# Performance work log

Measured on AMD Instinct MI355X. Metric: run time of the kernel, lower is better.

## Reference

```python
import jax, jax.numpy as jnp
import numpy as np

B, S, D = 8, 2048, 1024
H = 4
K = D // 2          # expand_k = 0.5 -> key dim 512
V = D               # expand_v = 1.0 -> value dim 1024
DK, DV = K // H, V // H   # 128, 256
LOW_RANK = 16
GATE_LOGIT_NORM = 16.0
EPS = 1e-5
MLP_H = 4 * D


def _layernorm(x, g, b):
    mu = jnp.mean(x, axis=-1, keepdims=True)
    var = jnp.mean(jnp.square(x - mu), axis=-1, keepdims=True)
    return (x - mu) * jax.lax.rsqrt(var + EPS) * g + b


def _rmsnorm(x, w):
    ms = jnp.mean(jnp.square(x), axis=-1, keepdims=True)
    return x * jax.lax.rsqrt(ms + EPS) * w


def _gla(xn, Wq, Wk, Wv, Wg, Wgk1, Wgk2, bgk, gnorm_w, Wo):
    # projections ([B,S,D] @ [D,*]); weights stored as [in, out]
    q = (xn @ Wq).reshape(B, S, H, DK) * (DK ** -0.5)
    k = (xn @ Wk).reshape(B, S, H, DK)
    v = (xn @ Wv).reshape(B, S, H, DV)
    gk = jax.nn.log_sigmoid(xn @ Wgk1 @ Wgk2 + bgk) / GATE_LOGIT_NORM
    gk = gk.reshape(B, S, H, DK)

    def step(state, inp):
        qt, kt, vt, gt = inp                     # [B,H,DK], [B,H,DK], [B,H,DV], [B,H,DK]
        state = jnp.exp(gt)[..., None] * state + kt[..., None] * vt[..., None, :]
        ot = jnp.einsum('bhk,bhkv->bhv', qt, state)
        return state, ot

    init = jnp.zeros((B, H, DK, DV), xn.dtype)
    xs = (q.transpose(1, 0, 2, 3), k.transpose(1, 0, 2, 3),
          v.transpose(1, 0, 2, 3), gk.transpose(1, 0, 2, 3))
    _, o = jax.lax.scan(step, init, xs)          # o: [S,B,H,DV]
    o = o.transpose(1, 0, 2, 3)                  # [B,S,H,DV]

    g = (xn @ Wg).reshape(B, S, H, DV)
    o = _rmsnorm(o, gnorm_w) * g * jax.nn.sigmoid(g)   # RMSNorm + swish output gate
    return o.reshape(B, S, V) @ Wo


def setup_inputs() -> dict:
    key = jax.random.key(0)
    ks = jax.random.split(key, 16)
    sd = 0.02
    return {
        'x': jax.random.normal(ks[0], (B, S, D), jnp.float32),
        'ln1_g': jnp.ones((D,), jnp.float32),
        'ln1_b': jnp.zeros((D,), jnp.float32),
        'Wq': jax.random.normal(ks[1], (D, K), jnp.float32) * sd,
        'Wk': jax.random.normal(ks[2], (D, K), jnp.float32) * sd,
        'Wv': jax.random.normal(ks[3], (D, V), jnp.float32) * sd,
        'Wg': jax.random.normal(ks[4], (D, V), jnp.float32) * sd,
        'Wgk1': jax.random.normal(ks[5], (D, LOW_RANK), jnp.float32) * sd,
        'Wgk2': jax.random.normal(ks[6], (LOW_RANK, K), jnp.float32) * sd,
        'bgk': jnp.zeros((K,), jnp.float32),
        'gnorm_w': jnp.ones((DV,), jnp.float32),
        'Wo': jax.random.normal(ks[7], (V, D), jnp.float32) * sd,
        'ln2_g': jnp.ones((D,), jnp.float32),
        'ln2_b': jnp.zeros((D,), jnp.float32),
        'W1': jax.random.normal(ks[8], (D, MLP_H), jnp.float32) * sd,
        'b1': jnp.zeros((MLP_H,), jnp.float32),
        'W2': jax.random.normal(ks[9], (MLP_H, D), jnp.float32) * sd,
        'b2': jnp.zeros((D,), jnp.float32),
    }


def reference(x, ln1_g, ln1_b, Wq, Wk, Wv, Wg, Wgk1, Wgk2, bgk, gnorm_w, Wo,
              ln2_g, ln2_b, W1, b1, W2, b2):
    # pre-norm GLA block, eval mode (dropout = identity)
    attn_out = _gla(_layernorm(x, ln1_g, ln1_b), Wq, Wk, Wv, Wg, Wgk1, Wgk2, bgk, gnorm_w, Wo)
    x = x + attn_out
    h = _layernorm(x, ln2_g, ln2_b)
    h = jax.nn.gelu(h @ W1 + b1, approximate=False) @ W2 + b2
    return x + h
```

## Files before the change

kernel.cpp:

```cpp
#include <hip/hip_runtime.h>
#include <stdint.h>


typedef unsigned short u16t;
typedef __attribute__((ext_vector_type(8))) short bf16x8;
typedef __attribute__((ext_vector_type(4))) float f32x4;
typedef __attribute__((ext_vector_type(4))) unsigned short u16x4;

__device__ __forceinline__ float bf2f(unsigned short u){ union{unsigned int i; float f;} v; v.i=((unsigned int)u)<<16; return v.f; }
__device__ __forceinline__ unsigned short f2bf(float f){ union{unsigned int i; float f;} v; v.f=f; unsigned int r=v.i+0x7FFFu+((v.i>>16)&1u); return (unsigned short)(r>>16); }
__device__ __forceinline__ f32x4 cvt4(u16x4 u){ f32x4 r; r[0]=bf2f(u[0]); r[1]=bf2f(u[1]); r[2]=bf2f(u[2]); r[3]=bf2f(u[3]); return r; }
__device__ __forceinline__ u16x4 pack4(f32x4 f){ u16x4 r; r[0]=f2bf(f[0]); r[1]=f2bf(f[1]); r[2]=f2bf(f[2]); r[3]=f2bf(f[3]); return r; }

__device__ __forceinline__ float gelu_f(float t){
  const float t3 = t*t*t;
  const float y = 2.3021183f*t + 0.10295465f*t3;
  const float e = __builtin_amdgcn_exp2f(y);
  return t - t*__builtin_amdgcn_rcpf(e + 1.f);
}

__device__ __forceinline__ void gload_lds16(const unsigned short* g, unsigned short* l)
{
  __builtin_amdgcn_global_load_lds(
      (const __attribute__((address_space(1))) unsigned int*)g,
      (__attribute__((address_space(3))) unsigned int*)l,
      16, 0, 0);
}

__global__ void k_transpose_multi(const float* __restrict__ Wq, const float* __restrict__ Wk,
                                  const float* __restrict__ Wv, const float* __restrict__ Wg,
                                  const float* __restrict__ Wo, const float* __restrict__ W1,
                                  const float* __restrict__ W2,
                                  unsigned short* __restrict__ WPT, unsigned short* __restrict__ WOT,
                                  unsigned short* __restrict__ W1T, unsigned short* __restrict__ W2T)
{
  __shared__ float tile[32][33];
  int bid = blockIdx.x;
  const float* src; unsigned short* dst; int Kin, N, nx;
  if      (bid < 512)  { src=Wq; dst=WPT;                          Kin=1024; N=512;  nx=16;  }
  else if (bid < 1024) { src=Wk; dst=WPT+(size_t)512*1024;         Kin=1024; N=512;  nx=16;  bid-=512;  }
  else if (bid < 2048) { src=Wv; dst=WPT+(size_t)1024*1024;        Kin=1024; N=1024; nx=32;  bid-=1024; }
  else if (bid < 3072) { src=Wg; dst=WPT+(size_t)2048*1024;        Kin=1024; N=1024; nx=32;  bid-=2048; }
  else if (bid < 4096) { src=Wo; dst=WOT;                          Kin=1024; N=1024; nx=32;  bid-=3072; }
  else if (bid < 8192) { src=W1; dst=W1T;                          Kin=1024; N=4096; nx=128; bid-=4096; }
  else                 { src=W2; dst=W2T;                          Kin=4096; N=1024; nx=32;  bid-=8192; }
  const int n0 = (bid % nx)*32, k0 = (bid / nx)*32;
  const int tx = threadIdx.x, ty = threadIdx.y;
  #pragma unroll
  for (int i = 0; i < 4; ++i)
    tile[ty + i*8][tx] = src[(size_t)(k0 + ty + i*8)*N + n0 + tx];
  __syncthreads();
  #pragma unroll
  for (int i = 0; i < 4; ++i)
    dst[(size_t)(n0 + ty + i*8)*Kin + k0 + tx] = f2bf(tile[tx][ty + i*8]);
}

__global__ void k_wgk(const float* __restrict__ Wgk1, const float* __restrict__ Wgk2, unsigned short* __restrict__ dstT)
{
  const int idx = blockIdx.x*256 + threadIdx.x;
  const int i = idx & 1023, j = idx >> 10;
  float s = 0.f;
  #pragma unroll
  for (int r = 0; r < 16; ++r) s += Wgk1[i*16 + r] * Wgk2[r*512 + j];
  dstT[(size_t)j*1024 + i] = f2bf(s);
}

__global__ void k_vtrans(const unsigned short* __restrict__ proj, unsigned short* __restrict__ vtg)
{
  __shared__ unsigned short tile[32][33];
  const int tt = blockIdx.x, dvt = blockIdx.y, bh = blockIdx.z;
  const int b = bh >> 2, h = bh & 3;
  const int tx = threadIdx.x, ty = threadIdx.y;
  #pragma unroll
  for (int i = 0; i < 4; ++i)
    tile[ty + i*8][tx] = proj[((size_t)b*2048 + tt*32 + ty + i*8)*3584 + 1024 + h*256 + dvt*32 + tx];
  __syncthreads();
  #pragma unroll
  for (int i = 0; i < 4; ++i)
    vtg[((size_t)bh*256 + dvt*32 + ty + i*8)*2048 + tt*32 + tx] = tile[tx][ty + i*8];
}

__global__ __launch_bounds__(256) void k_layernorm(const float* __restrict__ x, const float* __restrict__ g,
                                                   const float* __restrict__ b, unsigned short* __restrict__ out)
{
  const int row = blockIdx.x, tid = threadIdx.x;
  const float4 xv = *(const float4*)&x[(size_t)row*1024 + tid*4];
  float s  = xv.x + xv.y + xv.z + xv.w;
  float sq = xv.x*xv.x + xv.y*xv.y + xv.z*xv.z + xv.w*xv.w;
  #pragma unroll
  for (int o = 32; o > 0; o >>= 1) { s += __shfl_xor(s, o); sq += __shfl_xor(sq, o); }
  __shared__ float red[8];
  const int w = tid >> 6;
  if ((tid & 63) == 0) { red[w] = s; red[4 + w] = sq; }
  __syncthreads();
  s  = red[0] + red[1] + red[2] + red[3];
  sq = red[4] + red[5] + red[6] + red[7];
  const float mu = s * (1.f/1024.f);
  const float var = sq * (1.f/1024.f) - mu*mu;
  const float rs = rsqrtf(var + 1e-5f);
  float xe[4] = {xv.x, xv.y, xv.z, xv.w};
  u16x4 o4;
  #pragma unroll
  for (int i = 0; i < 4; ++i) {
    const int c = tid*4 + i;
    o4[i] = f2bf((xe[i] - mu) * rs * g[c] + b[c]);
  }
  *(u16x4*)&out[(size_t)row*1024 + tid*4] = o4;
}

template<int EPI>
__global__ __launch_bounds__(512, 2)
void gemm256(const unsigned short* __restrict__ A, const unsigned short* __restrict__ Bt,
             int N, int K,
             float* outF, unsigned short* outH,
             const float* resid, const float* bias)
{
  __shared__ __align__(16) unsigned short lds[65536];
  const int tid = threadIdx.x;
  const int lane = tid & 63, w = tid >> 6;
  const int wr = w >> 2, wc = w & 3;
  const int l15 = lane & 15, lq = lane >> 4;

  const int nwg = gridDim.x * gridDim.y;
  const int bid = blockIdx.y * gridDim.x + blockIdx.x;
  const int q = nwg >> 3, r = nwg & 7;
  const int xcd = bid & 7, lid = bid >> 3;
  const int sw = (xcd < r ? xcd*(q+1) : r*(q+1) + (xcd - r)*q) + lid;
  const int row0 = (sw / gridDim.x) * 256;
  const int col0 = (sw % gridDim.x) * 256;

  const int rA_ = tid >> 3;
  const int cswz = 8 * ((tid & 7) ^ (rA_ & 7));
  const unsigned short* baseA[2][2];
  const unsigned short* baseB[2][2];
  #pragma unroll
  for (int h = 0; h < 2; ++h)
    #pragma unroll
    for (int L = 0; L < 2; ++L) {
      baseA[h][L] = A  + (size_t)(row0 + h*128 + L*64 + rA_) * K + cswz;
      baseB[h][L] = Bt + (size_t)(col0 + h*128 + L*64 + rA_) * K + cswz;
    }

  const int NT = K >> 6;
  const int NI = NT >> 1;

  f32x4 acc[8][4];
  #pragma unroll
  for (int m = 0; m < 8; ++m)
    #pragma unroll
    for (int n = 0; n < 4; ++n) { acc[m][n][0]=0.f; acc[m][n][1]=0.f; acc[m][n][2]=0.f; acc[m][n][3]=0.f; }

  bf16x8 af[4][2];
  bf16x8 bfr[2][2][2];

  #define STAGE(CH, T)                                                         \
    {                                                                          \
      const int tt = ((T) < NT) ? (T) : (T) - 2;                               \
      const int dbase = (tt & 1) * 32768 + (CH) * 8192;                        \
      const int ktt = tt << 6;                                                 \
      _Pragma("unroll")                                                        \
      for (int L = 0; L < 2; ++L) {                                            \
        const unsigned short* gp =                                             \
            ((CH) < 2 ? baseA[(CH) & 1][L] : baseB[(CH) & 1][L]) + ktt;        \
        gload_lds16(gp, (unsigned short*)&lds[dbase + L*4096 + w*512]);        \
      }                                                                        \
    }

  #define DS_A(CB)                                                             \
    { _Pragma("unroll")                                                        \
      for (int mm = 0; mm < 4; ++mm) {                                         \
        const int rl = wr*64 + mm*16 + l15;                                    \
        const int co = (l15 & 7) * 8;                                          \
        af[mm][0] = *(const bf16x8*)&lds[(CB) + rl*64 + ((lq*8) ^ co)];        \
        af[mm][1] = *(const bf16x8*)&lds[(CB) + rl*64 + ((32 + lq*8) ^ co)];   \
      } }

  #define DS_B(CB, QN)                                                         \
    { _Pragma("unroll")                                                        \
      for (int nn = 0; nn < 2; ++nn) {                                         \
        const int rl = wc*32 + nn*16 + l15;                                    \
        const int co = (l15 & 7) * 8;                                          \
        bfr[QN][nn][0] = *(const bf16x8*)&lds[(CB) + (2+(QN))*8192 + rl*64 + ((lq*8) ^ co)];      \
        bfr[QN][nn][1] = *(const bf16x8*)&lds[(CB) + (2+(QN))*8192 + rl*64 + ((32 + lq*8) ^ co)]; \
      } }

  #define PRE_MFMA()                                                           \
    { __builtin_amdgcn_s_barrier();                                            \
      asm volatile("s_waitcnt lgkmcnt(0)" ::: "memory");                       \
      __builtin_amdgcn_sched_barrier(0); }

  #define MMA(QM, QN)                                                          \
    { __builtin_amdgcn_s_setprio(1);                                           \
      _Pragma("unroll")                                                        \
      for (int mm = 0; mm < 4; ++mm)                                           \
        _Pragma("unroll")                                                      \
        for (int nn = 0; nn < 2; ++nn) {                                       \
          acc[(QM)*4+mm][(QN)*2+nn] = __builtin_amdgcn_mfma_f32_16x16x32_bf16( \
              af[mm][0], bfr[QN][nn][0], acc[(QM)*4+mm][(QN)*2+nn], 0, 0, 0);  \
          acc[(QM)*4+mm][(QN)*2+nn] = __builtin_amdgcn_mfma_f32_16x16x32_bf16( \
              af[mm][1], bfr[QN][nn][1], acc[(QM)*4+mm][(QN)*2+nn], 0, 0, 0);  \
        }                                                                      \
      __builtin_amdgcn_s_setprio(0); }

  #define POSTW(VN)                                                            \
    { asm volatile("s_waitcnt vmcnt(" #VN ")" ::: "memory");                   \
      __builtin_amdgcn_sched_barrier(0);                                       \
      __builtin_amdgcn_s_barrier(); }

  #define POSTN() { __builtin_amdgcn_s_barrier(); }

  STAGE(0, 0); STAGE(2, 0); STAGE(1, 0); STAGE(3, 0); STAGE(0, 1); STAGE(2, 1);
  asm volatile("s_waitcnt vmcnt(8)" ::: "memory");
  __builtin_amdgcn_sched_barrier(0);
  __builtin_amdgcn_s_barrier();

  for (int i = 0; i < NI; ++i) {
    const int t0 = 2*i, t1 = 2*i + 1;
    DS_A(0); DS_B(0, 0); STAGE(1, t1);
    PRE_MFMA(); MMA(0, 0); POSTW(6);
    DS_B(0, 1); STAGE(3, t1);
    PRE_MFMA(); MMA(0, 1); POSTN();
    DS_A(8192); STAGE(0, t0 + 2);
    PRE_MFMA(); MMA(1, 0); POSTN();
    STAGE(2, t0 + 2);
    PRE_MFMA(); MMA(1, 1); POSTW(8);
    DS_A(32768); DS_B(32768, 0); STAGE(1, t0 + 2);
    PRE_MFMA(); MMA(0, 0); POSTW(6);
    DS_B(32768, 1); STAGE(3, t0 + 2);
    PRE_MFMA(); MMA(0, 1); POSTN();
    DS_A(32768 + 8192); STAGE(0, t1 + 2);
    PRE_MFMA(); MMA(1, 0); POSTN();
    STAGE(2, t1 + 2);
    PRE_MFMA(); MMA(1, 1); POSTW(8);
  }
  #undef STAGE
  #undef DS_A
  #undef DS_B
  #undef PRE_MFMA
  #undef MMA
  #undef POSTW
  #undef POSTN

  #pragma unroll
  for (int qm = 0; qm < 2; ++qm)
    #pragma unroll
    for (int mm = 0; mm < 4; ++mm)
      #pragma unroll
      for (int qn = 0; qn < 2; ++qn)
        #pragma unroll
        for (int nn = 0; nn < 2; ++nn)
          #pragma unroll
          for (int ii = 0; ii < 4; ++ii) {
            const int rr = row0 + qm*128 + wr*64 + mm*16 + lq*4 + ii;
            const int cc = col0 + qn*128 + wc*32 + nn*16 + l15;
            const size_t idx = (size_t)rr * N + cc;
            const float v = acc[qm*4+mm][qn*2+nn][ii];
            if constexpr (EPI == 0) {
              outH[idx] = f2bf(v);
            } else if constexpr (EPI == 1) {
              outF[idx] = v + resid[idx];
            } else if constexpr (EPI == 2) {
              outH[idx] = f2bf(gelu_f(v + bias[cc]));
            } else {
              outF[idx] = v + bias[cc] + resid[idx];
            }
          }
}

__global__ __launch_bounds__(128) void k_scanprep(const unsigned short* __restrict__ proj, const float* __restrict__ bgk,
                                                  unsigned short* __restrict__ qt, unsigned short* __restrict__ kt,
                                                  float* __restrict__ eac)
{
  const int c = blockIdx.x & 31, bh = blockIdx.x >> 5;
  const int b = bh >> 2, h = bh & 3;
  const int dk = threadIdx.x;
  const size_t tok0 = (size_t)b*2048 + c*64;
  const float bg = bgk[h*128 + dk];
  float A = 0.f, ea = 1.f;
  for (int t = 0; t < 64; ++t) {
    const size_t prow = (tok0 + t) * 3584;
    const float qv = bf2f(proj[prow + h*128 + dk]);
    const float kv = bf2f(proj[prow + 512 + h*128 + dk]);
    const float z = bf2f(proj[prow + 3072 + h*128 + dk]) + bg;
    const float az = fabsf(z);
    const float sp = fmaxf(-z, 0.f)
                   + 0.69314718f*__builtin_amdgcn_logf(1.f + __builtin_amdgcn_exp2f(-1.44269504f*az));
    A -= sp * 0.0625f;
    ea = __builtin_amdgcn_exp2f(A * 1.44269504f);
    const float em = __builtin_amdgcn_rcpf(ea);
    const size_t orow = ((size_t)bh*2048 + c*64 + t)*128 + dk;
    qt[orow] = f2bf(qv * ea * 0.08838834764831845f);
    kt[orow] = f2bf(kv * em);
  }
  eac[((size_t)bh*32 + c)*128 + dk] = ea;
}

__global__ __launch_bounds__(128) void k_seqstate(const unsigned short* __restrict__ kt,
                                                  const unsigned short* __restrict__ proj,
                                                  const float* __restrict__ eac,
                                                  unsigned short* __restrict__ sst)
{
  __shared__ __align__(16) unsigned short KVs[2][6144];
  const int bid = blockIdx.x;
  const int bh = bid >> 4, dks = (bid >> 3) & 1, dvs = bid & 7;
  const int b = bh >> 2, h = bh & 3;
  const int tid = threadIdx.x;
  const int w = tid >> 6;
  const int dkl = (tid >> 3) * 4, dv0 = (tid & 7) * 4;
  const int vcol0 = 1024 + h*256 + dvs*32;

  #define SSTAGE(C, BUF)                                                        \
    {                                                                           \
      const size_t tk0 = (size_t)bh*2048 + (size_t)(C)*64;                      \
      const size_t tv0 = (size_t)b*2048 + (size_t)(C)*64;                       \
      _Pragma("unroll")                                                         \
      for (int it = 0; it < 4; ++it) {                                          \
        const int e = it*1024 + tid*8; const int t = e >> 6, col = e & 63;      \
        gload_lds16(&kt[(tk0 + t)*128 + dks*64 + col],                          \
                    (unsigned short*)&KVs[BUF][it*1024 + w*512]);               \
      }                                                                         \
      _Pragma("unroll")                                                         \
      for (int it = 0; it < 2; ++it) {                                          \
        const int e = it*1024 + tid*8; const int t = e >> 5, j = e & 31;        \
        gload_lds16(&proj[(tv0 + t)*3584 + vcol0 + j],                          \
                    (unsigned short*)&KVs[BUF][4096 + it*1024 + w*512]);        \
      }                                                                         \
    }

  f32x4 acc4[4];
  #pragma unroll
  for (int i = 0; i < 4; ++i) { acc4[i][0]=0.f; acc4[i][1]=0.f; acc4[i][2]=0.f; acc4[i][3]=0.f; }

  SSTAGE(0, 0);
  asm volatile("s_waitcnt vmcnt(0)" ::: "memory");
  __builtin_amdgcn_sched_barrier(0);
  __syncthreads();

  for (int c = 0; c < 32; ++c) {
    const int buf = c & 1;
    if (c + 1 < 32) SSTAGE(c + 1, buf ^ 1);
    const size_t sb = ((size_t)bh*32 + c)*256;
    #pragma unroll
    for (int j = 0; j < 4; ++j) {
      u16x4 tj;
      tj[0]=f2bf(acc4[0][j]); tj[1]=f2bf(acc4[1][j]); tj[2]=f2bf(acc4[2][j]); tj[3]=f2bf(acc4[3][j]);
      *(u16x4*)&sst[(sb + dvs*32 + dv0 + j)*128 + dks*64 + dkl] = tj;
    }
    for (int t = 0; t < 64; ++t) {
      const f32x4 ka = cvt4(*(const u16x4*)&KVs[buf][t*64 + dkl]);
      const f32x4 vv = cvt4(*(const u16x4*)&KVs[buf][4096 + t*32 + dv0]);
      acc4[0] += vv * ka[0]; acc4[1] += vv * ka[1]; acc4[2] += vv * ka[2]; acc4[3] += vv * ka[3];
    }
    #pragma unroll
    for (int i = 0; i < 4; ++i)
      acc4[i] *= eac[((size_t)bh*32 + c)*128 + dks*64 + dkl + i];
    __syncthreads();
  }
  #undef SSTAGE
}

__global__ __launch_bounds__(512) void k_attn_out(const unsigned short* __restrict__ qt,
                                                  const unsigned short* __restrict__ kt,
                                                  const unsigned short* __restrict__ vtg,
                                                  const unsigned short* __restrict__ sst,
                                                  const unsigned short* __restrict__ proj,
                                                  const float* __restrict__ gnw,
                                                  unsigned short* __restrict__ og)
{
  __shared__ __align__(16) unsigned short SL[61440];
  __shared__ float ssq[64];
  const int c = blockIdx.x & 31, bh = blockIdx.x >> 5;
  const int b = bh >> 2, h = bh & 3;
  const int tid = threadIdx.x, lane = tid & 63, w = tid >> 6;
  const int wr = w >> 2, wc = w & 3;
  const int l15 = lane & 15, lq = lane >> 4;
  const size_t qk0 = (size_t)bh*2048 + c*64;
  const size_t tok0 = (size_t)b*2048 + c*64;
  const int key15 = (l15 & 7) << 3;

  if (tid < 64) ssq[tid] = 0.f;

  const int kc8 = (lane & 7) * 8;
  #pragma unroll
  for (int it = 0; it < 2; ++it) {
    const int o = it*4096 + w*512 + lane*8;
    const int ch = o >> 12, r = (o >> 6) & 63;
    gload_lds16(&kt[(qk0 + r)*128 + ch*64 + (kc8 ^ ((r & 7) << 3))],
                (unsigned short*)&SL[53248 + it*4096 + w*512]);
  }
  #pragma unroll
  for (int it = 0; it < 4; ++it) {
    const int o = it*4096 + w*512 + lane*8;
    const int dv = o >> 6;
    gload_lds16(&vtg[((size_t)bh*256 + dv)*2048 + c*64 + (kc8 ^ ((dv & 7) << 3))],
                (unsigned short*)&SL[4096 + it*4096 + w*512]);
  }
  #pragma unroll
  for (int it = 0; it < 8; ++it) {
    const int o = it*4096 + w*512 + lane*8;
    const int ch = o >> 14, dv = (o >> 6) & 255;
    gload_lds16(&sst[((size_t)(bh*32 + c)*256 + dv)*128 + ch*64 + (kc8 ^ ((dv & 7) << 3))],
                (unsigned short*)&SL[20480 + it*4096 + w*512]);
  }
  bf16x8 aq[2][4];
  #pragma unroll
  for (int mm = 0; mm < 2; ++mm)
    #pragma unroll
    for (int k4 = 0; k4 < 4; ++k4)
      aq[mm][k4] = *(const bf16x8*)&qt[(qk0 + wr*32 + mm*16 + l15)*128 + k4*32 + lq*8];

  __syncthreads();

  f32x4 accp[2];
  accp[0][0]=0.f; accp[0][1]=0.f; accp[0][2]=0.f; accp[0][3]=0.f;
  accp[1] = accp[0];
  #pragma unroll
  for (int k4 = 0; k4 < 4; ++k4) {
    const int ch = k4 >> 1, k0c = (k4 & 1) * 32;
    const bf16x8 bk = *(const bf16x8*)&SL[53248 + ch*4096 + (wc*16 + l15)*64 + ((k0c + lq*8) ^ key15)];
    accp[0] = __builtin_amdgcn_mfma_f32_16x16x32_bf16(aq[0][k4], bk, accp[0], 0, 0, 0);
    accp[1] = __builtin_amdgcn_mfma_f32_16x16x32_bf16(aq[1][k4], bk, accp[1], 0, 0, 0);
  }
  #pragma unroll
  for (int mm = 0; mm < 2; ++mm)
    #pragma unroll
    for (int i = 0; i < 4; ++i) {
      const int rg = wr*32 + mm*16 + lq*4 + i;
      const int cg = wc*16 + l15;
      SL[rg*64 + (cg ^ ((rg & 7) << 3))] = f2bf((cg <= rg) ? accp[mm][i] : 0.f);
    }
  __syncthreads();

  f32x4 acco[2][4];
  #pragma unroll
  for (int mm = 0; mm < 2; ++mm)
    #pragma unroll
    for (int nn = 0; nn < 4; ++nn) { acco[mm][nn][0]=0.f; acco[mm][nn][1]=0.f; acco[mm][nn][2]=0.f; acco[mm][nn][3]=0.f; }

  #pragma unroll
  for (int t4 = 0; t4 < 2; ++t4) {
    bf16x8 ap[2];
    #pragma unroll
    for (int mm = 0; mm < 2; ++mm) {
      const int r = wr*32 + mm*16 + l15;
      ap[mm] = *(const bf16x8*)&SL[r*64 + ((t4*32 + lq*8) ^ key15)];
    }
    #pragma unroll
    for (int nn = 0; nn < 4; ++nn) {
      const int dv = wc*64 + nn*16 + l15;
      const bf16x8 bv = *(const bf16x8*)&SL[4096 + dv*64 + ((t4*32 + lq*8) ^ key15)];
      acco[0][nn] = __builtin_amdgcn_mfma_f32_16x16x32_bf16(ap[0], bv, acco[0][nn], 0, 0, 0);
      acco[1][nn] = __builtin_amdgcn_mfma_f32_16x16x32_bf16(ap[1], bv, acco[1][nn], 0, 0, 0);
    }
  }
  #pragma unroll
  for (int k4 = 0; k4 < 4; ++k4) {
    const int ch = k4 >> 1, k0c = (k4 & 1) * 32;
    #pragma unroll
    for (int nn = 0; nn < 4; ++nn) {
      const int dv = wc*64 + nn*16 + l15;
      const bf16x8 bs = *(const bf16x8*)&SL[20480 + ch*16384 + dv*64 + ((k0c + lq*8) ^ key15)];
      acco[0][nn] = __builtin_amdgcn_mfma_f32_16x16x32_bf16(aq[0][k4], bs, acco[0][nn], 0, 0, 0);
      acco[1][nn] = __builtin_amdgcn_mfma_f32_16x16x32_bf16(aq[1][k4], bs, acco[1][nn], 0, 0, 0);
    }
  }

  #pragma unroll
  for (int mm = 0; mm < 2; ++mm) {
    float part[4];
    #pragma unroll
    for (int i = 0; i < 4; ++i) {
      float s = 0.f;
      #pragma unroll
      for (int nn = 0; nn < 4; ++nn) s += acco[mm][nn][i]*acco[mm][nn][i];
      s += __shfl_xor(s, 1); s += __shfl_xor(s, 2); s += __shfl_xor(s, 4); s += __shfl_xor(s, 8);
      part[i] = s;
    }
    if (l15 == 0) {
      #pragma unroll
      for (int i = 0; i < 4; ++i)
        atomicAdd(&ssq[wr*32 + mm*16 + lq*4 + i], part[i]);
    }
  }
  __syncthreads();

  #pragma unroll
  for (int mm = 0; mm < 2; ++mm)
    #pragma unroll
    for (int i = 0; i < 4; ++i) {
      const int rg = wr*32 + mm*16 + lq*4 + i;
      const float rs = rsqrtf(ssq[rg] * (1.f/256.f) + 1e-5f);
      const size_t token = tok0 + rg;
      #pragma unroll
      for (int nn = 0; nn < 4; ++nn) {
        const int dv = wc*64 + nn*16 + l15;
        const float gf = bf2f(proj[token*3584 + 2048 + h*256 + dv]);
        const float swv = gf * __builtin_amdgcn_rcpf(1.f + __builtin_amdgcn_exp2f(-1.44269504f*gf));
        og[token*1024 + h*256 + dv] = f2bf(acco[mm][nn][i] * rs * gnw[dv] * swv);
      }
    }
}

extern "C" void kernel_launch(void* const* d_in, const int* in_sizes, int n_in,
                              void* d_out, int out_size, void* d_ws, size_t ws_size,
                              hipStream_t stream)
{
  (void)in_sizes; (void)n_in; (void)out_size; (void)ws_size;
  const float* x    = (const float*)d_in[0];
  const float* ln1g = (const float*)d_in[1];
  const float* ln1b = (const float*)d_in[2];
  const float* Wq   = (const float*)d_in[3];
  const float* Wk   = (const float*)d_in[4];
  const float* Wv   = (const float*)d_in[5];
  const float* Wg   = (const float*)d_in[6];
  const float* Wgk1 = (const float*)d_in[7];
  const float* Wgk2 = (const float*)d_in[8];
  const float* bgk  = (const float*)d_in[9];
  const float* gnw  = (const float*)d_in[10];
  const float* Wo   = (const float*)d_in[11];
  const float* ln2g = (const float*)d_in[12];
  const float* ln2b = (const float*)d_in[13];
  const float* W1   = (const float*)d_in[14];
  const float* b1   = (const float*)d_in[15];
  const float* W2   = (const float*)d_in[16];
  const float* b2   = (const float*)d_in[17];
  float* out = (float*)d_out;
  char* ws = (char*)d_ws;

  u16t*  XN   = (u16t*)(ws + 0);
  u16t*  WPT  = (u16t*)(ws + 33554432);
  u16t*  WOT  = (u16t*)(ws + 40894464);
  u16t*  W1T  = (u16t*)(ws + 42991616);
  u16t*  W2T  = (u16t*)(ws + 51380224);
  u16t*  PROJ = (u16t*)(ws + 59768832);
  u16t*  QT   = (u16t*)(ws + 177209344);
  u16t*  KT   = (u16t*)(ws + 193986560);
  float* EAC  = (float*)(ws + 210763776);
  u16t*  VT   = (u16t*)(ws + 211288064);
  u16t*  H2   = (u16t*)(ws + 211288064);
  u16t*  OG   = (u16t*)(ws + 0);
  u16t*  HID  = PROJ;
  u16t*  SST  = (u16t*)d_out;

  k_transpose_multi<<<12288, dim3(32,8), 0, stream>>>(Wq, Wk, Wv, Wg, Wo, W1, W2, WPT, WOT, W1T, W2T);
  k_wgk<<<2048, 256, 0, stream>>>(Wgk1, Wgk2, WPT + (size_t)3072*1024);

  k_layernorm<<<16384, 256, 0, stream>>>(x, ln1g, ln1b, XN);
  gemm256<0><<<dim3(14,64), 512, 0, stream>>>(XN, WPT, 3584, 1024, nullptr, PROJ, nullptr, nullptr);
  k_vtrans<<<dim3(64,8,32), dim3(32,8), 0, stream>>>(PROJ, VT);
  k_scanprep<<<1024, 128, 0, stream>>>(PROJ, bgk, QT, KT, EAC);
  k_seqstate<<<512, 128, 0, stream>>>(KT, PROJ, EAC, SST);
  k_attn_out<<<1024, 512, 0, stream>>>(QT, KT, VT, SST, PROJ, gnw, OG);
  gemm256<1><<<dim3(4,64),  512, 0, stream>>>(OG, WOT, 1024, 1024, out, nullptr, x, nullptr);
  k_layernorm<<<16384, 256, 0, stream>>>(out, ln2g, ln2b, H2);
  gemm256<2><<<dim3(16,64), 512, 0, stream>>>(H2, W1T, 4096, 1024, nullptr, HID, nullptr, b1);
  gemm256<3><<<dim3(4,64),  512, 0, stream>>>(HID, W2T, 1024, 4096, out, nullptr, out, b2);
}
```

Baseline: 809.0 us.

## Compute chunk state recurrence with MFMA using pre-transposed K and V

The per-chunk inter-chunk state kernel is rewritten to use bf16 MFMA instructions instead of scalar FMA loops. The transpose kernel now also produces a time-major transposed copy of the decayed keys, so both operands can be streamed into XOR-swizzled LDS tiles with direct global-to-LDS loads and double buffering. Block size grows to 512 threads with fewer blocks. The cost is an extra transpose pass over K and an extra workspace buffer that aliases the normalized-input region.

```diff
diff --git a/kernel.cpp b/kernel.cpp
--- a/kernel.cpp
+++ b/kernel.cpp
@@ -10,7 +10,6 @@
 __device__ __forceinline__ float bf2f(unsigned short u){ union{unsigned int i; float f;} v; v.i=((unsigned int)u)<<16; return v.f; }
 __device__ __forceinline__ unsigned short f2bf(float f){ union{unsigned int i; float f;} v; v.f=f; unsigned int r=v.i+0x7FFFu+((v.i>>16)&1u); return (unsigned short)(r>>16); }
 __device__ __forceinline__ f32x4 cvt4(u16x4 u){ f32x4 r; r[0]=bf2f(u[0]); r[1]=bf2f(u[1]); r[2]=bf2f(u[2]); r[3]=bf2f(u[3]); return r; }
-__device__ __forceinline__ u16x4 pack4(f32x4 f){ u16x4 r; r[0]=f2bf(f[0]); r[1]=f2bf(f[1]); r[2]=f2bf(f[2]); r[3]=f2bf(f[3]); return r; }
 
 __device__ __forceinline__ float gelu_f(float t){
   const float t3 = t*t*t;
@@ -65,19 +64,32 @@
   dstT[(size_t)j*1024 + i] = f2bf(s);
 }
 
-__global__ void k_vtrans(const unsigned short* __restrict__ proj, unsigned short* __restrict__ vtg)
+__global__ void k_vtrans(const unsigned short* __restrict__ proj, const unsigned short* __restrict__ kt,
+                         unsigned short* __restrict__ vtg, unsigned short* __restrict__ ktt)
 {
   __shared__ unsigned short tile[32][33];
-  const int tt = blockIdx.x, dvt = blockIdx.y, bh = blockIdx.z;
+  const int tt = blockIdx.x, zz = blockIdx.y, bh = blockIdx.z;
   const int b = bh >> 2, h = bh & 3;
   const int tx = threadIdx.x, ty = threadIdx.y;
-  #pragma unroll
-  for (int i = 0; i < 4; ++i)
-    tile[ty + i*8][tx] = proj[((size_t)b*2048 + tt*32 + ty + i*8)*3584 + 1024 + h*256 + dvt*32 + tx];
-  __syncthreads();
-  #pragma unroll
-  for (int i = 0; i < 4; ++i)
-    vtg[((size_t)bh*256 + dvt*32 + ty + i*8)*2048 + tt*32 + tx] = tile[tx][ty + i*8];
+  if (zz < 8) {
+    const int dvt = zz;
+    #pragma unroll
+    for (int i = 0; i < 4; ++i)
+      tile[ty + i*8][tx] = proj[((size_t)b*2048 + tt*32 + ty + i*8)*3584 + 1024 + h*256 + dvt*32 + tx];
+    __syncthreads();
+    #pragma unroll
+    for (int i = 0; i < 4; ++i)
+      vtg[((size_t)bh*256 + dvt*32 + ty + i*8)*2048 + tt*32 + tx] = tile[tx][ty + i*8];
+  } else {
+    const int dkt = zz - 8;
+    #pragma unroll
+    for (int i = 0; i < 4; ++i)
+      tile[ty + i*8][tx] = kt[((size_t)bh*2048 + tt*32 + ty + i*8)*128 + dkt*32 + tx];
+    __syncthreads();
+    #pragma unroll
+    for (int i = 0; i < 4; ++i)
+      ktt[((size_t)bh*128 + dkt*32 + ty + i*8)*2048 + tt*32 + tx] = tile[tx][ty + i*8];
+  }
 }
 
 __global__ __launch_bounds__(256) void k_layernorm(const float* __restrict__ x, const float* __restrict__ g,
@@ -157,11 +169,11 @@
     {                                                                          \
       const int tt = ((T) < NT) ? (T) : (T) - 2;                               \
       const int dbase = (tt & 1) * 32768 + (CH) * 8192;                        \
-      const int ktt = tt << 6;                                                 \
+      const int ktt2 = tt << 6;                                                \
       _Pragma("unroll")                                                        \
       for (int L = 0; L < 2; ++L) {                                            \
         const unsigned short* gp =                                             \
-            ((CH) < 2 ? baseA[(CH) & 1][L] : baseB[(CH) & 1][L]) + ktt;        \
+            ((CH) < 2 ? baseA[(CH) & 1][L] : baseB[(CH) & 1][L]) + ktt2;       \
         gload_lds16(gp, (unsigned short*)&lds[dbase + L*4096 + w*512]);        \
       }                                                                        \
     }
@@ -295,66 +307,89 @@
   eac[((size_t)bh*32 + c)*128 + dk] = ea;
 }
 
-__global__ __launch_bounds__(128) void k_seqstate(const unsigned short* __restrict__ kt,
-                                                  const unsigned short* __restrict__ proj,
+__global__ __launch_bounds__(512) void k_seqstate(const unsigned short* __restrict__ ktt,
+                                                  const unsigned short* __restrict__ vtg,
                                                   const float* __restrict__ eac,
                                                   unsigned short* __restrict__ sst)
 {
-  __shared__ __align__(16) unsigned short KVs[2][6144];
+  __shared__ __align__(16) unsigned short SLq[16384];
   const int bid = blockIdx.x;
-  const int bh = bid >> 4, dks = (bid >> 3) & 1, dvs = bid & 7;
-  const int b = bh >> 2, h = bh & 3;
-  const int tid = threadIdx.x;
-  const int w = tid >> 6;
-  const int dkl = (tid >> 3) * 4, dv0 = (tid & 7) * 4;
-  const int vcol0 = 1024 + h*256 + dvs*32;
+  const int bh = bid >> 3, dks = (bid >> 2) & 1, dvs = bid & 3;
+  const int tid = threadIdx.x, lane = tid & 63, w = tid >> 6;
+  const int wr = w >> 2, wc = w & 3;
+  const int l15 = lane & 15, lq = lane >> 4;
+  const int kc8 = (lane & 7) * 8;
 
   #define SSTAGE(C, BUF)                                                        \
-    {                                                                           \
-      const size_t tk0 = (size_t)bh*2048 + (size_t)(C)*64;                      \
-      const size_t tv0 = (size_t)b*2048 + (size_t)(C)*64;                       \
-      _Pragma("unroll")                                                         \
-      for (int it = 0; it < 4; ++it) {                                          \
-        const int e = it*1024 + tid*8; const int t = e >> 6, col = e & 63;      \
-        gload_lds16(&kt[(tk0 + t)*128 + dks*64 + col],                          \
-                    (unsigned short*)&KVs[BUF][it*1024 + w*512]);               \
-      }                                                                         \
-      _Pragma("unroll")                                                         \
-      for (int it = 0; it < 2; ++it) {                                          \
-        const int e = it*1024 + tid*8; const int t = e >> 5, j = e & 31;        \
-        gload_lds16(&proj[(tv0 + t)*3584 + vcol0 + j],                          \
-                    (unsigned short*)&KVs[BUF][4096 + it*1024 + w*512]);        \
-      }                                                                         \
-    }
-
-  f32x4 acc4[4];
-  #pragma unroll
-  for (int i = 0; i < 4; ++i) { acc4[i][0]=0.f; acc4[i][1]=0.f; acc4[i][2]=0.f; acc4[i][3]=0.f; }
+    { { const int o = w*512 + lane*8;                                           \
+        const int dkl = o >> 6;                                                 \
+        gload_lds16(&ktt[((size_t)bh*128 + dks*64 + dkl)*2048 + (C)*64 + (kc8 ^ ((dkl & 7) << 3))], \
+                    (unsigned short*)&SLq[(BUF)*8192 + w*512]); }                \
+      { const int o = w*512 + lane*8;                                           \
+        const int dvl = o >> 6;                                                 \
+        gload_lds16(&vtg[((size_t)bh*256 + dvs*64 + dvl)*2048 + (C)*64 + (kc8 ^ ((dvl & 7) << 3))], \
+                    (unsigned short*)&SLq[(BUF)*8192 + 4096 + w*512]); } }
+
+  f32x4 acc[2];
+  acc[0][0]=0.f; acc[0][1]=0.f; acc[0][2]=0.f; acc[0][3]=0.f;
+  acc[1] = acc[0];
 
   SSTAGE(0, 0);
   asm volatile("s_waitcnt vmcnt(0)" ::: "memory");
   __builtin_amdgcn_sched_barrier(0);
-  __syncthreads();
+  __builtin_amdgcn_s_barrier();
 
   for (int c = 0; c < 32; ++c) {
     const int buf = c & 1;
-    if (c + 1 < 32) SSTAGE(c + 1, buf ^ 1);
-    const size_t sb = ((size_t)bh*32 + c)*256;
-    #pragma unroll
-    for (int j = 0; j < 4; ++j) {
+    if (c + 1 < 32) {
+      SSTAGE(c + 1, buf ^ 1);
+      asm volatile("s_waitcnt vmcnt(2)" ::: "memory");
+    } else {
+      asm volatile("s_waitcnt vmcnt(0)" ::: "memory");
+    }
+    __builtin_amdgcn_sched_barrier(0);
+    __builtin_amdgcn_s_barrier();
+
+    const size_t srow = (((size_t)bh*32 + c)*256 + dvs*64 + wc*16 + l15)*128;
+    #pragma unroll
+    for (int mm = 0; mm < 2; ++mm) {
       u16x4 tj;
-      tj[0]=f2bf(acc4[0][j]); tj[1]=f2bf(acc4[1][j]); tj[2]=f2bf(acc4[2][j]); tj[3]=f2bf(acc4[3][j]);
-      *(u16x4*)&sst[(sb + dvs*32 + dv0 + j)*128 + dks*64 + dkl] = tj;
-    }
-    for (int t = 0; t < 64; ++t) {
-      const f32x4 ka = cvt4(*(const u16x4*)&KVs[buf][t*64 + dkl]);
-      const f32x4 vv = cvt4(*(const u16x4*)&KVs[buf][4096 + t*32 + dv0]);
-      acc4[0] += vv * ka[0]; acc4[1] += vv * ka[1]; acc4[2] += vv * ka[2]; acc4[3] += vv * ka[3];
-    }
-    #pragma unroll
-    for (int i = 0; i < 4; ++i)
-      acc4[i] *= eac[((size_t)bh*32 + c)*128 + dks*64 + dkl + i];
-    __syncthreads();
+      tj[0]=f2bf(acc[mm][0]); tj[1]=f2bf(acc[mm][1]); tj[2]=f2bf(acc[mm][2]); tj[3]=f2bf(acc[mm][3]);
+      *(u16x4*)&sst[srow + dks*64 + wr*32 + mm*16 + lq*4] = tj;
+    }
+    f32x4 ev[2];
+    #pragma unroll
+    for (int mm = 0; mm < 2; ++mm)
+      ev[mm] = *(const f32x4*)&eac[(size_t)(bh*32 + c)*128 + dks*64 + wr*32 + mm*16 + lq*4];
+
+    const int base = buf*8192;
+    bf16x8 afr[2][2], bfrg[2];
+    #pragma unroll
+    for (int mm = 0; mm < 2; ++mm) {
+      const int rl = wr*32 + mm*16 + l15;
+      const int co = (rl & 7) << 3;
+      afr[mm][0] = *(const bf16x8*)&SLq[base + rl*64 + ((lq*8) ^ co)];
+      afr[mm][1] = *(const bf16x8*)&SLq[base + rl*64 + ((32 + lq*8) ^ co)];
+    }
+    {
+      const int dvl = wc*16 + l15;
+      const int co = (dvl & 7) << 3;
+      bfrg[0] = *(const bf16x8*)&SLq[base + 4096 + dvl*64 + ((lq*8) ^ co)];
+      bfrg[1] = *(const bf16x8*)&SLq[base + 4096 + dvl*64 + ((32 + lq*8) ^ co)];
+    }
+    asm volatile("s_waitcnt lgkmcnt(0)" ::: "memory");
+    __builtin_amdgcn_sched_barrier(0);
+    #pragma unroll
+    for (int k4 = 0; k4 < 2; ++k4)
+      #pragma unroll
+      for (int mm = 0; mm < 2; ++mm)
+        acc[mm] = __builtin_amdgcn_mfma_f32_16x16x32_bf16(afr[mm][k4], bfrg[k4], acc[mm], 0, 0, 0);
+    #pragma unroll
+    for (int mm = 0; mm < 2; ++mm)
+      #pragma unroll
+      for (int i = 0; i < 4; ++i)
+        acc[mm][i] *= ev[mm][i];
+    __builtin_amdgcn_s_barrier();
   }
   #undef SSTAGE
 }
@@ -528,6 +563,8 @@
   char* ws = (char*)d_ws;
 
   u16t*  XN   = (u16t*)(ws + 0);
+  u16t*  KTT  = (u16t*)(ws + 0);
+  u16t*  OG   = (u16t*)(ws + 0);
   u16t*  WPT  = (u16t*)(ws + 33554432);
   u16t*  WOT  = (u16t*)(ws + 40894464);
   u16t*  W1T  = (u16t*)(ws + 42991616);
@@ -538,7 +575,6 @@
   float* EAC  = (float*)(ws + 210763776);
   u16t*  VT   = (u16t*)(ws + 211288064);
   u16t*  H2   = (u16t*)(ws + 211288064);
-  u16t*  OG   = (u16t*)(ws + 0);
   u16t*  HID  = PROJ;
   u16t*  SST  = (u16t*)d_out;
 
@@ -547,9 +583,9 @@
 
   k_layernorm<<<16384, 256, 0, stream>>>(x, ln1g, ln1b, XN);
   gemm256<0><<<dim3(14,64), 512, 0, stream>>>(XN, WPT, 3584, 1024, nullptr, PROJ, nullptr, nullptr);
-  k_vtrans<<<dim3(64,8,32), dim3(32,8), 0, stream>>>(PROJ, VT);
   k_scanprep<<<1024, 128, 0, stream>>>(PROJ, bgk, QT, KT, EAC);
-  k_seqstate<<<512, 128, 0, stream>>>(KT, PROJ, EAC, SST);
+  k_vtrans<<<dim3(64,12,32), dim3(32,8), 0, stream>>>(PROJ, KT, VT, KTT);
+  k_seqstate<<<256, 512, 0, stream>>>(KTT, VT, EAC, SST);
   k_attn_out<<<1024, 512, 0, stream>>>(QT, KT, VT, SST, PROJ, gnw, OG);
   gemm256<1><<<dim3(4,64),  512, 0, stream>>>(OG, WOT, 1024, 1024, out, nullptr, x, nullptr);
   k_layernorm<<<16384, 256, 0, stream>>>(out, ln2g, ln2b, H2);
```

Measured after the change: 692.2 us. 1.17x faster.
